# Performance work log

Measured on AMD Instinct MI355X. Metric: run time of the kernel, lower is better.

The kernel has to match this reference:

```python
import jax, jax.numpy as jnp
import numpy as np

N = 50000   # nodes
E = 400000  # edges
IN = 64     # input feature dim
H = 4       # heads (layers 1-2)
C = 128     # hidden channels per head
NEG_SLOPE = 0.2


def gat_conv(x, W, a_src, a_dst, b, src, dst, num_nodes):
    """PyG-style GATConv (add_self_loops=False, dropout inactive / eval mode).
    x: [N, F_in]; W: [F_in, H*C]; a_src/a_dst: [H, C]; b: [H*C].
    Returns concat-over-heads output [N, H*C]."""
    h = (x @ W).reshape(num_nodes, a_src.shape[0], a_src.shape[1])  # [N,H,C]
    alpha_s = jnp.einsum('nhc,hc->nh', h, a_src)  # [N,H]
    alpha_d = jnp.einsum('nhc,hc->nh', h, a_dst)  # [N,H]
    e = jax.nn.leaky_relu(alpha_s[src] + alpha_d[dst], NEG_SLOPE)  # [E,H]
    # numerically-stable segment softmax over incoming edges of each dst node
    m = jax.ops.segment_max(e, dst, num_segments=num_nodes)       # [N,H]
    m = jnp.where(jnp.isfinite(m), m, 0.0)                        # empty segments
    p = jnp.exp(e - m[dst])                                       # [E,H]
    denom = jax.ops.segment_sum(p, dst, num_segments=num_nodes)   # [N,H]
    alpha = p / (denom[dst] + 1e-16)                              # [E,H]
    # message = alpha * h[src], scatter-add into dst
    out = jax.ops.segment_sum(alpha[:, :, None] * h[src], dst,
                              num_segments=num_nodes)             # [N,H,C]
    return out.reshape(num_nodes, -1) + b


def setup_inputs() -> dict:
    key = jax.random.key(0)
    ks = jax.random.split(key, 16)
    s = 0.1  # weight scale for stability
    inp = {
        'x': jax.random.normal(ks[0], (N, IN), dtype=jnp.float32),
        'edge_index': jax.random.randint(ks[1], (2, E), 0, N, dtype=jnp.int64),
        # layer 1: 64 -> H*C
        'W1': s * jax.random.normal(ks[2], (IN, H * C), dtype=jnp.float32),
        'a_src1': s * jax.random.normal(ks[3], (H, C), dtype=jnp.float32),
        'a_dst1': s * jax.random.normal(ks[4], (H, C), dtype=jnp.float32),
        'b1': jnp.zeros((H * C,), dtype=jnp.float32),
        # layer 2: H*C -> H*C
        'W2': s * jax.random.normal(ks[5], (H * C, H * C), dtype=jnp.float32),
        'a_src2': s * jax.random.normal(ks[6], (H, C), dtype=jnp.float32),
        'a_dst2': s * jax.random.normal(ks[7], (H, C), dtype=jnp.float32),
        'b2': jnp.zeros((H * C,), dtype=jnp.float32),
        # layer 3: H*C -> C (heads=1)
        'W3': s * jax.random.normal(ks[8], (H * C, C), dtype=jnp.float32),
        'a_src3': s * jax.random.normal(ks[9], (1, C), dtype=jnp.float32),
        'a_dst3': s * jax.random.normal(ks[10], (1, C), dtype=jnp.float32),
        'b3': jnp.zeros((C,), dtype=jnp.float32),
    }
    return inp


def reference(x, edge_index, W1, a_src1, a_dst1, b1, W2, a_src2, a_dst2, b2,
              W3, a_src3, a_dst3, b3):
    src, dst = edge_index[0], edge_index[1]
    h = jax.nn.elu(gat_conv(x, W1, a_src1, a_dst1, b1, src, dst, N))
    h = jax.nn.elu(gat_conv(h, W2, a_src2, a_dst2, b2, src, dst, N))
    h = jax.nn.elu(gat_conv(h, W3, a_src3, a_dst3, b3, src, dst, N))
    return h  # [N, C]
```

## Files before the change

### kernel.cpp

```cpp
#include <hip/hip_runtime.h>
#include <math.h>


#define LRELU_SLOPE 0.2f
#define MPAD 50048

typedef __attribute__((ext_vector_type(8))) short short8;
typedef __attribute__((ext_vector_type(4))) float f32x4;

__device__ __forceinline__ float bf2f(unsigned short u) {
    return __uint_as_float(((unsigned int)u) << 16);
}
__device__ __forceinline__ unsigned short f2bf(float f) {
    unsigned int u = __float_as_uint(f);
    unsigned int r = u + 0x7FFFu + ((u >> 16) & 1u);
    return (unsigned short)(r >> 16);
}
__device__ __forceinline__ void load16_to_lds(const void* g, void* l) {
    __builtin_amdgcn_global_load_lds(
        (const __attribute__((address_space(1))) void*)g,
        (__attribute__((address_space(3))) void*)l, 16, 0, 0);
}
__device__ __forceinline__ float lrelu(float e) {
    return e > 0.f ? e : LRELU_SLOPE * e;
}


__global__ void count_deg_kernel(const int* __restrict__ dst, int* __restrict__ counts, int E) {
    int e = blockIdx.x * blockDim.x + threadIdx.x;
    if (e < E) atomicAdd(&counts[dst[e]], 1);
}

__global__ __launch_bounds__(1024) void scan1_kernel(const int* __restrict__ counts,
                                                     int* __restrict__ row_ptr,
                                                     int* __restrict__ partial, int n) {
    __shared__ int wsum[16];
    const int t = threadIdx.x;
    const int lane = t & 63, w = t >> 6;
    const int i = blockIdx.x * 1024 + t;
    int v = (i < n) ? counts[i] : 0;
    int s = v;
    #pragma unroll
    for (int off = 1; off < 64; off <<= 1) {
        int u = __shfl_up(s, off);
        if (lane >= off) s += u;
    }
    if (lane == 63) wsum[w] = s;
    __syncthreads();
    if (w == 0 && lane < 16) {
        int tv = wsum[lane];
        #pragma unroll
        for (int off = 1; off < 16; off <<= 1) {
            int u = __shfl_up(tv, off);
            if (lane >= off) tv += u;
        }
        wsum[lane] = tv;
    }
    __syncthreads();
    int incl = s + (w > 0 ? wsum[w - 1] : 0);
    if (i < n) row_ptr[i + 1] = incl;
    if (t == 0) partial[blockIdx.x] = wsum[15];
}

__global__ void scan2_kernel(int* __restrict__ partial, int nb) {
    int lane = threadIdx.x;
    int v = (lane < nb) ? partial[lane] : 0;
    int s = v;
    #pragma unroll
    for (int off = 1; off < 64; off <<= 1) {
        int u = __shfl_up(s, off);
        if (lane >= off) s += u;
    }
    if (lane < nb) partial[lane] = s - v;
}

__global__ __launch_bounds__(1024) void scan3_kernel(int* __restrict__ row_ptr,
                                                     const int* __restrict__ partial, int n) {
    const int i = blockIdx.x * 1024 + threadIdx.x;
    if (i < n) row_ptr[i + 1] += partial[blockIdx.x];
    if (i == 0) row_ptr[0] = 0;
}

__global__ void init_cursor_kernel(const int* __restrict__ row_ptr, int* __restrict__ cursor, int n) {
    int i = blockIdx.x * blockDim.x + threadIdx.x;
    if (i < n) cursor[i] = row_ptr[i];
}

__global__ void fill_csr_kernel(const int* __restrict__ src, const int* __restrict__ dst,
                                int* __restrict__ cursor, int* __restrict__ csr_src,
                                int* __restrict__ csr_dst, int E) {
    int e = blockIdx.x * blockDim.x + threadIdx.x;
    if (e < E) {
        int d = dst[e];
        int pos = atomicAdd(&cursor[d], 1);
        csr_src[pos] = src[e];
        csr_dst[pos] = d;
    }
}


__global__ void cast_f32_bf16_kernel(const float* __restrict__ in, unsigned short* __restrict__ out,
                                     size_t n) {
    size_t i = (size_t)blockIdx.x * blockDim.x + threadIdx.x;
    if (i < n) out[i] = f2bf(in[i]);
}

__global__ void transpose_cast_kernel(const float* __restrict__ W, unsigned short* __restrict__ Wt,
                                      int K, int Nw) {
    int i = blockIdx.x * blockDim.x + threadIdx.x;
    if (i < K * Nw) {
        int k = i / Nw, nn = i % Nw;
        Wt[(size_t)nn * K + k] = f2bf(W[i]);
    }
}


__global__ __launch_bounds__(256) void gemm_mfma_kernel(
    const unsigned short* __restrict__ A,
    const unsigned short* __restrict__ Bt,
    unsigned short* __restrict__ C,
    const float* __restrict__ a_src,
    const float* __restrict__ a_dst,
    float* __restrict__ als,
    float* __restrict__ ald,
    int M, int N, int K, int H)
{
    __shared__ short As[2 * 128 * 32];
    __shared__ short Bs[2 * 128 * 32];
    const int t = threadIdx.x;
    const int w = t >> 6, lane = t & 63;
    const int wr = w >> 1, wc = w & 1;

    const int nwg = gridDim.x * gridDim.y;
    const int wg  = blockIdx.x + gridDim.x * blockIdx.y;
    const int qch = nwg >> 3, rch = nwg & 7;
    const int xcd = wg & 7, pos = wg >> 3;
    const int lg  = (xcd < rch ? xcd * (qch + 1) : rch * (qch + 1) + (xcd - rch) * qch) + pos;
    const int bx  = lg % gridDim.x;
    const int by  = lg / gridDim.x;

    const int rowBase = by * 128;
    const int colBase = bx * 128;
    const int q = lane >> 4;
    const int r16 = lane & 15;
    const int qs = (q ^ ((r16 >> 1) & 3)) * 8;

    f32x4 acc[4][4] = {};

    const int sRow = t >> 2;
    const int sOff = ((t & 3) ^ ((sRow >> 1) & 3)) * 8;

    const int NT = K >> 5;
    auto stage = [&](int kt, int b) {
        const int koff = kt * 32 + sOff;
        #pragma unroll
        for (int rr = 0; rr < 2; ++rr) {
            const unsigned short* gA = A + (size_t)(rowBase + rr * 64 + sRow) * K + koff;
            load16_to_lds(gA, (char*)As + b * 8192 + rr * 4096 + w * 1024);
            const unsigned short* gB = Bt + (size_t)(colBase + rr * 64 + sRow) * K + koff;
            load16_to_lds(gB, (char*)Bs + b * 8192 + rr * 4096 + w * 1024);
        }
    };

    stage(0, 0);
    __syncthreads();

    for (int kt = 0; kt < NT; ++kt) {
        const int cur = kt & 1;
        if (kt + 1 < NT) stage(kt + 1, cur ^ 1);

        const short* Ab = As + cur * 4096;
        const short* Bb = Bs + cur * 4096;
        short8 af[4], bfr[4];
        #pragma unroll
        for (int m = 0; m < 4; ++m)
            af[m] = *(const short8*)&Ab[(wr * 64 + m * 16 + r16) * 32 + qs];
        #pragma unroll
        for (int n = 0; n < 4; ++n)
            bfr[n] = *(const short8*)&Bb[(wc * 64 + n * 16 + r16) * 32 + qs];
        #pragma unroll
        for (int m = 0; m < 4; ++m)
            #pragma unroll
            for (int n = 0; n < 4; ++n)
                acc[m][n] = __builtin_amdgcn_mfma_f32_16x16x32_bf16(af[m], bfr[n], acc[m][n], 0, 0, 0);

        __syncthreads();
    }

    float asv[4], adv[4];
    #pragma unroll
    for (int n = 0; n < 4; ++n) {
        int col = colBase + wc * 64 + n * 16 + r16;
        asv[n] = a_src[col];
        adv[n] = a_dst[col];
    }
    const int head = bx;

    float* red = (float*)As;

    #pragma unroll
    for (int m = 0; m < 4; ++m) {
        #pragma unroll
        for (int r = 0; r < 4; ++r) {
            const int rowl = wr * 64 + m * 16 + q * 4 + r;
            const int gr = rowBase + rowl;
            float ps = 0.f, pd = 0.f;
            #pragma unroll
            for (int n = 0; n < 4; ++n) {
                ps += acc[m][n][r] * asv[n];
                pd += acc[m][n][r] * adv[n];
            }
            #pragma unroll
            for (int off = 8; off >= 1; off >>= 1) {
                ps += __shfl_xor(ps, off);
                pd += __shfl_xor(pd, off);
            }
            if (r16 == 0) {
                red[wc * 128 + rowl] = ps;
                red[256 + wc * 128 + rowl] = pd;
            }
            if (gr < M) {
                #pragma unroll
                for (int n = 0; n < 4; ++n)
                    C[(size_t)gr * N + colBase + wc * 64 + n * 16 + r16] = f2bf(acc[m][n][r]);
            }
        }
    }
    __syncthreads();
    if (t < 128) {
        const int gr = rowBase + t;
        if (gr < M) {
            als[(size_t)gr * H + head] = red[t] + red[128 + t];
            ald[(size_t)gr * H + head] = red[256 + t] + red[384 + t];
        }
    }
}


template <int H>
__global__ __launch_bounds__(256) void edge_w_kernel(
    const int* __restrict__ csr_src, const int* __restrict__ csr_dst,
    const float* __restrict__ als, const float* __restrict__ ald,
    float* __restrict__ wplane, int E)
{
    int p = blockIdx.x * 256 + threadIdx.x;
    if (p >= E) return;
    int s = csr_src[p], d = csr_dst[p];
    if constexpr (H == 4) {
        float4 a = *(const float4*)&als[(size_t)s * 4];
        float4 b = *(const float4*)&ald[(size_t)d * 4];
        wplane[p]               = __expf(lrelu(a.x + b.x));
        wplane[(size_t)E + p]   = __expf(lrelu(a.y + b.y));
        wplane[2*(size_t)E + p] = __expf(lrelu(a.z + b.z));
        wplane[3*(size_t)E + p] = __expf(lrelu(a.w + b.w));
    } else {
        wplane[p] = __expf(lrelu(als[s] + ald[d]));
    }
}


__global__ __launch_bounds__(256) void gather4_kernel(
    const unsigned short* __restrict__ hfeat,
    const float* __restrict__ wplane,
    const int* __restrict__ row_ptr, const int* __restrict__ csr_src,
    const float* __restrict__ bias, unsigned short* __restrict__ out,
    int E, int n_nodes)
{
    const int lane = threadIdx.x & 63;
    const int wv = threadIdx.x >> 6;
    const int n = blockIdx.x * 4 + wv;
    if (n >= n_nodes) return;
    const int head = lane >> 4;
    const int li = lane & 15;
    const int grpBase = lane & ~15;

    const int start = row_ptr[n];
    const int deg = row_ptr[n + 1] - start;
    const float* wpl = wplane + (size_t)head * E;

    float acc[8] = {};
    float wsum = 0.f;
    for (int base = 0; base < deg; base += 16) {
        const int cnt = min(16, deg - base);
        int s_l = 0; float w_l = 0.f;
        if (li < cnt) {
            s_l = csr_src[start + base + li];
            w_l = wpl[start + base + li];
            wsum += w_l;
        }
        for (int e = 0; e < cnt; ++e) {
            const int s = __shfl(s_l, grpBase + e);
            const float a = __shfl(w_l, grpBase + e);
            short8 v = *(const short8*)(hfeat + (size_t)s * 512 + lane * 8);
            #pragma unroll
            for (int j = 0; j < 8; ++j) acc[j] += a * bf2f((unsigned short)v[j]);
        }
    }

    #pragma unroll
    for (int off = 8; off >= 1; off >>= 1) wsum += __shfl_xor(wsum, off);
    const float sc = (deg > 0) ? 1.f / wsum : 0.f;

    float ov[8];
    #pragma unroll
    for (int j = 0; j < 8; ++j) {
        float o = acc[j] * sc + bias[lane * 8 + j];
        ov[j] = o > 0.f ? o : expm1f(o);
    }
    short8 v;
    #pragma unroll
    for (int j = 0; j < 8; ++j) v[j] = (short)f2bf(ov[j]);
    *(short8*)&out[(size_t)n * 512 + lane * 8] = v;
}


__global__ __launch_bounds__(256) void gather1_kernel(
    const unsigned short* __restrict__ hfeat,
    const float* __restrict__ wplane,
    const int* __restrict__ row_ptr, const int* __restrict__ csr_src,
    const float* __restrict__ bias, float* __restrict__ out, int n_nodes)
{
    const int lane = threadIdx.x & 63;
    const int wv = threadIdx.x >> 6;
    const int n = blockIdx.x * 4 + wv;
    if (n >= n_nodes) return;
    const int qid = lane >> 4;
    const int ql = lane & 15;

    const int start = row_ptr[n];
    const int deg = row_ptr[n + 1] - start;

    float acc[8] = {};
    float wsum = 0.f;
    for (int base = 0; base < deg; base += 64) {
        const int cnt = min(64, deg - base);
        int s_l = 0; float w_l = 0.f;
        if (lane < cnt) {
            s_l = csr_src[start + base + lane];
            w_l = wplane[start + base + lane];
            wsum += w_l;
        }
        for (int e = 0; e < cnt; e += 4) {
            const int idx = e + qid;
            const int idxc = idx < cnt ? idx : 0;
            const int s = __shfl(s_l, idxc);
            const float aw = __shfl(w_l, idxc);
            const float a = idx < cnt ? aw : 0.f;
            short8 v = *(const short8*)(hfeat + (size_t)s * 128 + ql * 8);
            #pragma unroll
            for (int j = 0; j < 8; ++j) acc[j] += a * bf2f((unsigned short)v[j]);
        }
    }

    #pragma unroll
    for (int off = 32; off >= 1; off >>= 1) wsum += __shfl_xor(wsum, off);
    const float sc = (deg > 0) ? 1.f / wsum : 0.f;

    #pragma unroll
    for (int j = 0; j < 8; ++j) {
        acc[j] += __shfl_xor(acc[j], 16);
        acc[j] += __shfl_xor(acc[j], 32);
    }

    if (qid == 0) {
        float tmp[8];
        #pragma unroll
        for (int j = 0; j < 8; ++j) {
            float o = acc[j] * sc + bias[ql * 8 + j];
            tmp[j] = o > 0.f ? o : expm1f(o);
        }
        float4 o0 = {tmp[0], tmp[1], tmp[2], tmp[3]};
        float4 o1 = {tmp[4], tmp[5], tmp[6], tmp[7]};
        float* op = out + (size_t)n * 128 + ql * 8;
        *(float4*)op = o0;
        *(float4*)(op + 4) = o1;
    }
}


extern "C" void kernel_launch(void* const* d_in, const int* in_sizes, int n_in,
                              void* d_out, int out_size, void* d_ws, size_t ws_size,
                              hipStream_t stream) {
    const float* x   = (const float*)d_in[0];
    const int*   ei  = (const int*)d_in[1];
    const float* W1  = (const float*)d_in[2];
    const float* as1 = (const float*)d_in[3];
    const float* ad1 = (const float*)d_in[4];
    const float* b1  = (const float*)d_in[5];
    const float* W2  = (const float*)d_in[6];
    const float* as2 = (const float*)d_in[7];
    const float* ad2 = (const float*)d_in[8];
    const float* b2  = (const float*)d_in[9];
    const float* W3  = (const float*)d_in[10];
    const float* as3 = (const float*)d_in[11];
    const float* ad3 = (const float*)d_in[12];
    const float* b3  = (const float*)d_in[13];

    const int N = in_sizes[0] / 64;
    const int E = in_sizes[1] / 2;
    const int HC = 512;

    const int* src = ei;
    const int* dst = ei + E;

    size_t off = 0;
    auto carve = [&](size_t bytes) -> void* {
        void* p = (char*)d_ws + off;
        off += (bytes + 255) & ~(size_t)255;
        return p;
    };
    unsigned short* x_bf    = (unsigned short*)carve((size_t)MPAD * 64 * 2);
    unsigned short* feat_bf = (unsigned short*)carve((size_t)MPAD * HC * 2);
    unsigned short* h_bf    = (unsigned short*)carve((size_t)N * HC * 2);
    unsigned short* W1t     = (unsigned short*)carve((size_t)512 * 64 * 2);
    unsigned short* W2t     = (unsigned short*)carve((size_t)512 * 512 * 2);
    unsigned short* W3t     = (unsigned short*)carve((size_t)128 * 512 * 2);
    float* stats  = (float*)carve((size_t)N * 8 * sizeof(float));
    float* als    = stats;
    float* ald    = stats + (size_t)N * 4;
    float* wplane = (float*)carve((size_t)4 * E * sizeof(float));
    int*   counts = (int*)carve((size_t)N * sizeof(int));
    int*   row_ptr= (int*)carve((size_t)(N + 1) * sizeof(int));
    int*   cursor = (int*)carve((size_t)N * sizeof(int));
    int*   csr_src= (int*)carve((size_t)E * sizeof(int));
    int*   csr_dst= (int*)carve((size_t)E * sizeof(int));
    int*   partial= (int*)carve(64 * sizeof(int));
    (void)ws_size;

    const int nb = (N + 1023) / 1024;

    hipMemsetAsync(counts, 0, (size_t)N * sizeof(int), stream);
    count_deg_kernel<<<(E + 255) / 256, 256, 0, stream>>>(dst, counts, E);
    scan1_kernel<<<nb, 1024, 0, stream>>>(counts, row_ptr, partial, N);
    scan2_kernel<<<1, 64, 0, stream>>>(partial, nb);
    scan3_kernel<<<nb, 1024, 0, stream>>>(row_ptr, partial, N);
    init_cursor_kernel<<<(N + 255) / 256, 256, 0, stream>>>(row_ptr, cursor, N);
    fill_csr_kernel<<<(E + 255) / 256, 256, 0, stream>>>(src, dst, cursor, csr_src, csr_dst, E);

    cast_f32_bf16_kernel<<<((size_t)N * 64 + 255) / 256, 256, 0, stream>>>(x, x_bf, (size_t)N * 64);
    transpose_cast_kernel<<<(64 * 512 + 255) / 256, 256, 0, stream>>>(W1, W1t, 64, 512);
    transpose_cast_kernel<<<(512 * 512 + 255) / 256, 256, 0, stream>>>(W2, W2t, 512, 512);
    transpose_cast_kernel<<<(512 * 128 + 255) / 256, 256, 0, stream>>>(W3, W3t, 512, 128);

    const int rowTiles = (N + 127) / 128;
    const int aggBlocks = (N + 3) / 4;
    const int edgeBlocks = (E + 255) / 256;

    gemm_mfma_kernel<<<dim3(4, rowTiles), 256, 0, stream>>>(x_bf, W1t, h_bf, as1, ad1,
                                                            als, ald, N, 512, 64, 4);
    edge_w_kernel<4><<<edgeBlocks, 256, 0, stream>>>(csr_src, csr_dst, als, ald, wplane, E);
    gather4_kernel<<<aggBlocks, 256, 0, stream>>>(h_bf, wplane, row_ptr, csr_src,
                                                  b1, feat_bf, E, N);

    gemm_mfma_kernel<<<dim3(4, rowTiles), 256, 0, stream>>>(feat_bf, W2t, h_bf, as2, ad2,
                                                            als, ald, N, 512, 512, 4);
    edge_w_kernel<4><<<edgeBlocks, 256, 0, stream>>>(csr_src, csr_dst, als, ald, wplane, E);
    gather4_kernel<<<aggBlocks, 256, 0, stream>>>(h_bf, wplane, row_ptr, csr_src,
                                                  b2, feat_bf, E, N);

    gemm_mfma_kernel<<<dim3(1, rowTiles), 256, 0, stream>>>(feat_bf, W3t, h_bf, as3, ad3,
                                                            als, ald, N, 128, 512, 1);
    edge_w_kernel<1><<<edgeBlocks, 256, 0, stream>>>(csr_src, csr_dst, als, ald, wplane, E);
    gather1_kernel<<<aggBlocks, 256, 0, stream>>>(h_bf, wplane, row_ptr, csr_src,
                                                  b3, (float*)d_out, N);
}
```

Baseline: 383.2 us.

## Reorder layer-1 GAT as aggregate-then-project using folded attention weights

Layer 1 now folds W1 into the attention vectors, so the per-node attention logits come straight from the 64-dim input. It then aggregates the raw 64-dim inputs per head and runs a small GEMM with fused bias and ELU afterwards. This replaces gathering 512-wide projected features with gathering 64-wide inputs, which cuts edge-gather traffic for the first layer. Edge weights are also stored as interleaved float4 per edge instead of separate head planes. The cost is an extra aggregated buffer and a per-head GEMM, and the logits now use fp32 x while the features use bf16, so rounding differs slightly from before.

```diff
diff --git a/kernel.cpp b/kernel.cpp
--- a/kernel.cpp
+++ b/kernel.cpp
@@ -111,6 +111,244 @@
     if (i < K * Nw) {
         int k = i / Nw, nn = i % Nw;
         Wt[(size_t)nn * K + k] = f2bf(W[i]);
+    }
+}
+
+
+__global__ __launch_bounds__(256) void ws1_kernel(const float* __restrict__ W1,
+                                                  const float* __restrict__ as1,
+                                                  const float* __restrict__ ad1,
+                                                  float* __restrict__ ws) {
+    const int t = threadIdx.x;
+    const int h = t >> 6, k = t & 63;
+    float ss = 0.f, sd = 0.f;
+    for (int c = 0; c < 128; ++c) {
+        float wv = W1[k * 512 + h * 128 + c];
+        ss += wv * as1[h * 128 + c];
+        sd += wv * ad1[h * 128 + c];
+    }
+    ws[h * 64 + k] = ss;
+    ws[256 + h * 64 + k] = sd;
+}
+
+
+__global__ __launch_bounds__(256) void als1_kernel(const float* __restrict__ x,
+                                                   const float* __restrict__ ws,
+                                                   float* __restrict__ als,
+                                                   float* __restrict__ ald, int n_nodes) {
+    const int lane = threadIdx.x & 63;
+    const int wv = threadIdx.x >> 6;
+    const int n = blockIdx.x * 4 + wv;
+    if (n >= n_nodes) return;
+    const float xv = x[(size_t)n * 64 + lane];
+    float d0 = xv * ws[lane],        d1 = xv * ws[64 + lane];
+    float d2 = xv * ws[128 + lane],  d3 = xv * ws[192 + lane];
+    float e0 = xv * ws[256 + lane],  e1 = xv * ws[320 + lane];
+    float e2 = xv * ws[384 + lane],  e3 = xv * ws[448 + lane];
+    #pragma unroll
+    for (int off = 32; off >= 1; off >>= 1) {
+        d0 += __shfl_xor(d0, off); d1 += __shfl_xor(d1, off);
+        d2 += __shfl_xor(d2, off); d3 += __shfl_xor(d3, off);
+        e0 += __shfl_xor(e0, off); e1 += __shfl_xor(e1, off);
+        e2 += __shfl_xor(e2, off); e3 += __shfl_xor(e3, off);
+    }
+    if (lane == 0) {
+        float4 a = {d0, d1, d2, d3};
+        float4 b = {e0, e1, e2, e3};
+        *(float4*)&als[(size_t)n * 4] = a;
+        *(float4*)&ald[(size_t)n * 4] = b;
+    }
+}
+
+
+__global__ __launch_bounds__(256) void edge_w4_kernel(
+    const int* __restrict__ csr_src, const int* __restrict__ csr_dst,
+    const float* __restrict__ als, const float* __restrict__ ald,
+    float4* __restrict__ wplane4, int E)
+{
+    int p = blockIdx.x * 256 + threadIdx.x;
+    if (p >= E) return;
+    int s = csr_src[p], d = csr_dst[p];
+    float4 a = *(const float4*)&als[(size_t)s * 4];
+    float4 b = *(const float4*)&ald[(size_t)d * 4];
+    float4 o;
+    o.x = __expf(lrelu(a.x + b.x));
+    o.y = __expf(lrelu(a.y + b.y));
+    o.z = __expf(lrelu(a.z + b.z));
+    o.w = __expf(lrelu(a.w + b.w));
+    wplane4[p] = o;
+}
+
+__global__ __launch_bounds__(256) void edge_w1_kernel(
+    const int* __restrict__ csr_src, const int* __restrict__ csr_dst,
+    const float* __restrict__ als, const float* __restrict__ ald,
+    float* __restrict__ wplane, int E)
+{
+    int p = blockIdx.x * 256 + threadIdx.x;
+    if (p >= E) return;
+    wplane[p] = __expf(lrelu(als[csr_src[p]] + ald[csr_dst[p]]));
+}
+
+
+__global__ __launch_bounds__(256) void gatherx_kernel(
+    const unsigned short* __restrict__ x_bf,
+    const float4* __restrict__ wplane4,
+    const int* __restrict__ row_ptr, const int* __restrict__ csr_src,
+    unsigned short* __restrict__ xagg,
+    int n_nodes)
+{
+    const int lane = threadIdx.x & 63;
+    const int wv = threadIdx.x >> 6;
+    const int n = blockIdx.x * 4 + wv;
+    if (n >= n_nodes) return;
+    const int g = lane >> 3;
+    const int j = lane & 7;
+
+    const int start = row_ptr[n];
+    const int deg = row_ptr[n + 1] - start;
+
+    float acc[4][8] = {};
+    float asum[4] = {};
+
+    for (int base = 0; base < deg; base += 8) {
+        const int idx = base + g;
+        const bool ok = idx < deg;
+        const int p = start + (ok ? idx : 0);
+        const int s = csr_src[p];
+        float4 a4 = wplane4[p];
+        if (!ok) { a4.x = 0.f; a4.y = 0.f; a4.z = 0.f; a4.w = 0.f; }
+        short8 v = *(const short8*)(x_bf + (size_t)s * 64 + j * 8);
+        asum[0] += a4.x; asum[1] += a4.y; asum[2] += a4.z; asum[3] += a4.w;
+        #pragma unroll
+        for (int jj = 0; jj < 8; ++jj) {
+            const float xv = bf2f((unsigned short)v[jj]);
+            acc[0][jj] += a4.x * xv;
+            acc[1][jj] += a4.y * xv;
+            acc[2][jj] += a4.z * xv;
+            acc[3][jj] += a4.w * xv;
+        }
+    }
+
+    #pragma unroll
+    for (int h = 0; h < 4; ++h) {
+        asum[h] += __shfl_xor(asum[h], 8);
+        asum[h] += __shfl_xor(asum[h], 16);
+        asum[h] += __shfl_xor(asum[h], 32);
+        #pragma unroll
+        for (int jj = 0; jj < 8; ++jj) {
+            acc[h][jj] += __shfl_xor(acc[h][jj], 8);
+            acc[h][jj] += __shfl_xor(acc[h][jj], 16);
+            acc[h][jj] += __shfl_xor(acc[h][jj], 32);
+        }
+    }
+
+    if (lane < 32) {
+        const int h = g;
+        float sc = 0.f;
+        if (deg > 0) {
+            float av = (h == 0) ? asum[0] : (h == 1) ? asum[1] : (h == 2) ? asum[2] : asum[3];
+            sc = 1.f / av;
+        }
+        short8 o;
+        #pragma unroll
+        for (int jj = 0; jj < 8; ++jj) {
+            float val = ((h == 0) ? acc[0][jj] : (h == 1) ? acc[1][jj]
+                        : (h == 2) ? acc[2][jj] : acc[3][jj]) * sc;
+            o[jj] = (short)f2bf(val);
+        }
+        *(short8*)&xagg[(size_t)n * 256 + h * 64 + j * 8] = o;
+    }
+}
+
+
+__global__ __launch_bounds__(256) void gemm_out_kernel(
+    const unsigned short* __restrict__ A,
+    const unsigned short* __restrict__ Bt,
+    const float* __restrict__ bias,
+    unsigned short* __restrict__ Cout,
+    int M)
+{
+    __shared__ short As[2 * 128 * 32];
+    __shared__ short Bs[2 * 128 * 32];
+    const int t = threadIdx.x;
+    const int w = t >> 6, lane = t & 63;
+    const int wr = w >> 1, wc = w & 1;
+
+    const int nwg = gridDim.x * gridDim.y;
+    const int wg  = blockIdx.x + gridDim.x * blockIdx.y;
+    const int qch = nwg >> 3, rch = nwg & 7;
+    const int xcd = wg & 7, pos = wg >> 3;
+    const int lg  = (xcd < rch ? xcd * (qch + 1) : rch * (qch + 1) + (xcd - rch) * qch) + pos;
+    const int bx  = lg % gridDim.x;
+    const int by  = lg / gridDim.x;
+
+    const int rowBase = by * 128;
+    const int head = bx;
+    const int colBase = bx * 128;
+    const int q = lane >> 4;
+    const int r16 = lane & 15;
+    const int qs = (q ^ ((r16 >> 1) & 3)) * 8;
+
+    f32x4 acc[4][4] = {};
+
+    const int sRow = t >> 2;
+    const int sOff = ((t & 3) ^ ((sRow >> 1) & 3)) * 8;
+
+    auto stage = [&](int kt, int b) {
+        const int koff = kt * 32 + sOff;
+        #pragma unroll
+        for (int rr = 0; rr < 2; ++rr) {
+            const unsigned short* gA = A + (size_t)(rowBase + rr * 64 + sRow) * 256 + head * 64 + koff;
+            load16_to_lds(gA, (char*)As + b * 8192 + rr * 4096 + w * 1024);
+            const unsigned short* gB = Bt + (size_t)(colBase + rr * 64 + sRow) * 64 + koff;
+            load16_to_lds(gB, (char*)Bs + b * 8192 + rr * 4096 + w * 1024);
+        }
+    };
+
+    stage(0, 0);
+    __syncthreads();
+
+    #pragma unroll
+    for (int kt = 0; kt < 2; ++kt) {
+        const int cur = kt & 1;
+        if (kt + 1 < 2) stage(kt + 1, cur ^ 1);
+
+        const short* Ab = As + cur * 4096;
+        const short* Bb = Bs + cur * 4096;
+        short8 af[4], bfr[4];
+        #pragma unroll
+        for (int m = 0; m < 4; ++m)
+            af[m] = *(const short8*)&Ab[(wr * 64 + m * 16 + r16) * 32 + qs];
+        #pragma unroll
+        for (int n = 0; n < 4; ++n)
+            bfr[n] = *(const short8*)&Bb[(wc * 64 + n * 16 + r16) * 32 + qs];
+        #pragma unroll
+        for (int m = 0; m < 4; ++m)
+            #pragma unroll
+            for (int n = 0; n < 4; ++n)
+                acc[m][n] = __builtin_amdgcn_mfma_f32_16x16x32_bf16(af[m], bfr[n], acc[m][n], 0, 0, 0);
+
+        __syncthreads();
+    }
+
+    float bv[4];
+    #pragma unroll
+    for (int n = 0; n < 4; ++n) bv[n] = bias[colBase + wc * 64 + n * 16 + r16];
+
+    #pragma unroll
+    for (int m = 0; m < 4; ++m) {
+        #pragma unroll
+        for (int r = 0; r < 4; ++r) {
+            const int gr = rowBase + wr * 64 + m * 16 + q * 4 + r;
+            if (gr < M) {
+                #pragma unroll
+                for (int n = 0; n < 4; ++n) {
+                    float o = acc[m][n][r] + bv[n];
+                    o = o > 0.f ? o : expm1f(o);
+                    Cout[(size_t)gr * 512 + colBase + wc * 64 + n * 16 + r16] = f2bf(o);
+                }
+            }
+        }
     }
 }
 
@@ -237,34 +475,12 @@
 }
 
 
-template <int H>
-__global__ __launch_bounds__(256) void edge_w_kernel(
-    const int* __restrict__ csr_src, const int* __restrict__ csr_dst,
-    const float* __restrict__ als, const float* __restrict__ ald,
-    float* __restrict__ wplane, int E)
-{
-    int p = blockIdx.x * 256 + threadIdx.x;
-    if (p >= E) return;
-    int s = csr_src[p], d = csr_dst[p];
-    if constexpr (H == 4) {
-        float4 a = *(const float4*)&als[(size_t)s * 4];
-        float4 b = *(const float4*)&ald[(size_t)d * 4];
-        wplane[p]               = __expf(lrelu(a.x + b.x));
-        wplane[(size_t)E + p]   = __expf(lrelu(a.y + b.y));
-        wplane[2*(size_t)E + p] = __expf(lrelu(a.z + b.z));
-        wplane[3*(size_t)E + p] = __expf(lrelu(a.w + b.w));
-    } else {
-        wplane[p] = __expf(lrelu(als[s] + ald[d]));
-    }
-}
-
-
 __global__ __launch_bounds__(256) void gather4_kernel(
     const unsigned short* __restrict__ hfeat,
-    const float* __restrict__ wplane,
+    const float4* __restrict__ wplane4,
     const int* __restrict__ row_ptr, const int* __restrict__ csr_src,
     const float* __restrict__ bias, unsigned short* __restrict__ out,
-    int E, int n_nodes)
+    int n_nodes)
 {
     const int lane = threadIdx.x & 63;
     const int wv = threadIdx.x >> 6;
@@ -276,7 +492,6 @@
 
     const int start = row_ptr[n];
     const int deg = row_ptr[n + 1] - start;
-    const float* wpl = wplane + (size_t)head * E;
 
     float acc[8] = {};
     float wsum = 0.f;
@@ -285,7 +500,8 @@
         int s_l = 0; float w_l = 0.f;
         if (li < cnt) {
             s_l = csr_src[start + base + li];
-            w_l = wpl[start + base + li];
+            float4 w4 = wplane4[start + base + li];
+            w_l = (head == 0) ? w4.x : (head == 1) ? w4.y : (head == 2) ? w4.z : w4.w;
             wsum += w_l;
         }
         for (int e = 0; e < cnt; ++e) {
@@ -412,13 +628,16 @@
     unsigned short* x_bf    = (unsigned short*)carve((size_t)MPAD * 64 * 2);
     unsigned short* feat_bf = (unsigned short*)carve((size_t)MPAD * HC * 2);
     unsigned short* h_bf    = (unsigned short*)carve((size_t)N * HC * 2);
+    unsigned short* xagg    = (unsigned short*)carve((size_t)MPAD * 256 * 2);
     unsigned short* W1t     = (unsigned short*)carve((size_t)512 * 64 * 2);
     unsigned short* W2t     = (unsigned short*)carve((size_t)512 * 512 * 2);
     unsigned short* W3t     = (unsigned short*)carve((size_t)128 * 512 * 2);
     float* stats  = (float*)carve((size_t)N * 8 * sizeof(float));
     float* als    = stats;
     float* ald    = stats + (size_t)N * 4;
-    float* wplane = (float*)carve((size_t)4 * E * sizeof(float));
+    float4* wplane4 = (float4*)carve((size_t)E * sizeof(float4));
+    float* wplane1  = (float*)carve((size_t)E * sizeof(float));
+    float* ws     = (float*)carve(512 * sizeof(float));
     int*   counts = (int*)carve((size_t)N * sizeof(int));
     int*   row_ptr= (int*)carve((size_t)(N + 1) * sizeof(int));
     int*   cursor = (int*)carve((size_t)N * sizeof(int));
@@ -441,26 +660,26 @@
     transpose_cast_kernel<<<(64 * 512 + 255) / 256, 256, 0, stream>>>(W1, W1t, 64, 512);
     transpose_cast_kernel<<<(512 * 512 + 255) / 256, 256, 0, stream>>>(W2, W2t, 512, 512);
     transpose_cast_kernel<<<(512 * 128 + 255) / 256, 256, 0, stream>>>(W3, W3t, 512, 128);
+    ws1_kernel<<<1, 256, 0, stream>>>(W1, as1, ad1, ws);
 
     const int rowTiles = (N + 127) / 128;
     const int aggBlocks = (N + 3) / 4;
     const int edgeBlocks = (E + 255) / 256;
 
-    gemm_mfma_kernel<<<dim3(4, rowTiles), 256, 0, stream>>>(x_bf, W1t, h_bf, as1, ad1,
-                                                            als, ald, N, 512, 64, 4);
-    edge_w_kernel<4><<<edgeBlocks, 256, 0, stream>>>(csr_src, csr_dst, als, ald, wplane, E);
-    gather4_kernel<<<aggBlocks, 256, 0, stream>>>(h_bf, wplane, row_ptr, csr_src,
-                                                  b1, feat_bf, E, N);
+    als1_kernel<<<aggBlocks, 256, 0, stream>>>(x, ws, als, ald, N);
+    edge_w4_kernel<<<edgeBlocks, 256, 0, stream>>>(csr_src, csr_dst, als, ald, wplane4, E);
+    gatherx_kernel<<<aggBlocks, 256, 0, stream>>>(x_bf, wplane4, row_ptr, csr_src, xagg, N);
+    gemm_out_kernel<<<dim3(4, rowTiles), 256, 0, stream>>>(xagg, W1t, b1, feat_bf, N);
 
     gemm_mfma_kernel<<<dim3(4, rowTiles), 256, 0, stream>>>(feat_bf, W2t, h_bf, as2, ad2,
                                                             als, ald, N, 512, 512, 4);
-    edge_w_kernel<4><<<edgeBlocks, 256, 0, stream>>>(csr_src, csr_dst, als, ald, wplane, E);
-    gather4_kernel<<<aggBlocks, 256, 0, stream>>>(h_bf, wplane, row_ptr, csr_src,
-                                                  b2, feat_bf, E, N);
+    edge_w4_kernel<<<edgeBlocks, 256, 0, stream>>>(csr_src, csr_dst, als, ald, wplane4, E);
+    gather4_kernel<<<aggBlocks, 256, 0, stream>>>(h_bf, wplane4, row_ptr, csr_src,
+                                                  b2, feat_bf, N);
 
     gemm_mfma_kernel<<<dim3(1, rowTiles), 256, 0, stream>>>(feat_bf, W3t, h_bf, as3, ad3,
                                                             als, ald, N, 128, 512, 1);
-    edge_w_kernel<1><<<edgeBlocks, 256, 0, stream>>>(csr_src, csr_dst, als, ald, wplane, E);
-    gather1_kernel<<<aggBlocks, 256, 0, stream>>>(h_bf, wplane, row_ptr, csr_src,
+    edge_w1_kernel<<<edgeBlocks, 256, 0, stream>>>(csr_src, csr_dst, als, ald, wplane1, E);
+    gather1_kernel<<<aggBlocks, 256, 0, stream>>>(h_bf, wplane1, row_ptr, csr_src,
                                                   b3, (float*)d_out, N);
 }
```

Result: slower. 402.0 us (+4.9%).

## Fuse edge-weight computation into gather kernels and merge preprocessing launches

Applied to the files above, without the earlier changes.

Removes the separate edge_w kernels and their wplane buffer, so each gather now computes the exp(leaky_relu(als[src]+ald[dst])) weights inline from per-node scores. The cast, transpose and counts-zeroing launches are folded into one prep kernel, and cursor initialisation moves into the scan3 kernel, so csr_dst is no longer built. This cuts kernel launches and avoids writing and re-reading the per-edge weight planes. In exchange the gather recomputes exp per head per edge and does scattered reads into als.

```diff
diff --git a/kernel.cpp b/kernel.cpp
--- a/kernel.cpp
+++ b/kernel.cpp
@@ -23,6 +23,39 @@
 }
 __device__ __forceinline__ float lrelu(float e) {
     return e > 0.f ? e : LRELU_SLOPE * e;
+}
+
+
+__global__ __launch_bounds__(256) void prep_kernel(
+    const float* __restrict__ x, const float* __restrict__ W1,
+    const float* __restrict__ W2, const float* __restrict__ W3,
+    unsigned short* __restrict__ x_bf, unsigned short* __restrict__ W1t,
+    unsigned short* __restrict__ W2t, unsigned short* __restrict__ W3t,
+    int* __restrict__ counts, int N)
+{
+    int i = blockIdx.x * 256 + threadIdx.x;
+    const int nx = N * 64;
+    if (i < nx) { x_bf[i] = f2bf(x[i]); return; }
+    i -= nx;
+    if (i < 64 * 512) {
+        int k = i / 512, nn = i % 512;
+        W1t[nn * 64 + k] = f2bf(W1[i]);
+        return;
+    }
+    i -= 64 * 512;
+    if (i < 512 * 512) {
+        int k = i / 512, nn = i % 512;
+        W2t[nn * 512 + k] = f2bf(W2[i]);
+        return;
+    }
+    i -= 512 * 512;
+    if (i < 512 * 128) {
+        int k = i / 128, nn = i % 128;
+        W3t[(size_t)nn * 512 + k] = f2bf(W3[i]);
+        return;
+    }
+    i -= 512 * 128;
+    if (i < N) counts[i] = 0;
 }
 
 
@@ -74,43 +107,26 @@
     if (lane < nb) partial[lane] = s - v;
 }
 
-__global__ __launch_bounds__(1024) void scan3_kernel(int* __restrict__ row_ptr,
-                                                     const int* __restrict__ partial, int n) {
+__global__ __launch_bounds__(1024) void scan3c_kernel(int* __restrict__ row_ptr,
+                                                      const int* __restrict__ partial,
+                                                      const int* __restrict__ counts,
+                                                      int* __restrict__ cursor, int n) {
     const int i = blockIdx.x * 1024 + threadIdx.x;
-    if (i < n) row_ptr[i + 1] += partial[blockIdx.x];
+    if (i < n) {
+        int rp1 = row_ptr[i + 1] + partial[blockIdx.x];
+        row_ptr[i + 1] = rp1;
+        cursor[i] = rp1 - counts[i];
+    }
     if (i == 0) row_ptr[0] = 0;
 }
 
-__global__ void init_cursor_kernel(const int* __restrict__ row_ptr, int* __restrict__ cursor, int n) {
-    int i = blockIdx.x * blockDim.x + threadIdx.x;
-    if (i < n) cursor[i] = row_ptr[i];
-}
-
 __global__ void fill_csr_kernel(const int* __restrict__ src, const int* __restrict__ dst,
-                                int* __restrict__ cursor, int* __restrict__ csr_src,
-                                int* __restrict__ csr_dst, int E) {
+                                int* __restrict__ cursor, int* __restrict__ csr_src, int E) {
     int e = blockIdx.x * blockDim.x + threadIdx.x;
     if (e < E) {
         int d = dst[e];
         int pos = atomicAdd(&cursor[d], 1);
         csr_src[pos] = src[e];
-        csr_dst[pos] = d;
-    }
-}
-
-
-__global__ void cast_f32_bf16_kernel(const float* __restrict__ in, unsigned short* __restrict__ out,
-                                     size_t n) {
-    size_t i = (size_t)blockIdx.x * blockDim.x + threadIdx.x;
-    if (i < n) out[i] = f2bf(in[i]);
-}
-
-__global__ void transpose_cast_kernel(const float* __restrict__ W, unsigned short* __restrict__ Wt,
-                                      int K, int Nw) {
-    int i = blockIdx.x * blockDim.x + threadIdx.x;
-    if (i < K * Nw) {
-        int k = i / Nw, nn = i % Nw;
-        Wt[(size_t)nn * K + k] = f2bf(W[i]);
     }
 }
 
@@ -237,34 +253,12 @@
 }
 
 
-template <int H>
-__global__ __launch_bounds__(256) void edge_w_kernel(
-    const int* __restrict__ csr_src, const int* __restrict__ csr_dst,
+__global__ __launch_bounds__(256) void gather4f_kernel(
+    const unsigned short* __restrict__ hfeat,
     const float* __restrict__ als, const float* __restrict__ ald,
-    float* __restrict__ wplane, int E)
-{
-    int p = blockIdx.x * 256 + threadIdx.x;
-    if (p >= E) return;
-    int s = csr_src[p], d = csr_dst[p];
-    if constexpr (H == 4) {
-        float4 a = *(const float4*)&als[(size_t)s * 4];
-        float4 b = *(const float4*)&ald[(size_t)d * 4];
-        wplane[p]               = __expf(lrelu(a.x + b.x));
-        wplane[(size_t)E + p]   = __expf(lrelu(a.y + b.y));
-        wplane[2*(size_t)E + p] = __expf(lrelu(a.z + b.z));
-        wplane[3*(size_t)E + p] = __expf(lrelu(a.w + b.w));
-    } else {
-        wplane[p] = __expf(lrelu(als[s] + ald[d]));
-    }
-}
-
-
-__global__ __launch_bounds__(256) void gather4_kernel(
-    const unsigned short* __restrict__ hfeat,
-    const float* __restrict__ wplane,
     const int* __restrict__ row_ptr, const int* __restrict__ csr_src,
     const float* __restrict__ bias, unsigned short* __restrict__ out,
-    int E, int n_nodes)
+    int n_nodes)
 {
     const int lane = threadIdx.x & 63;
     const int wv = threadIdx.x >> 6;
@@ -276,7 +270,7 @@
 
     const int start = row_ptr[n];
     const int deg = row_ptr[n + 1] - start;
-    const float* wpl = wplane + (size_t)head * E;
+    const float aldv = ald[(size_t)n * 4 + head];
 
     float acc[8] = {};
     float wsum = 0.f;
@@ -285,7 +279,8 @@
         int s_l = 0; float w_l = 0.f;
         if (li < cnt) {
             s_l = csr_src[start + base + li];
-            w_l = wpl[start + base + li];
+            float e = als[(size_t)s_l * 4 + head] + aldv;
+            w_l = __expf(lrelu(e));
             wsum += w_l;
         }
         for (int e = 0; e < cnt; ++e) {
@@ -314,9 +309,9 @@
 }
 
 
-__global__ __launch_bounds__(256) void gather1_kernel(
+__global__ __launch_bounds__(256) void gather1f_kernel(
     const unsigned short* __restrict__ hfeat,
-    const float* __restrict__ wplane,
+    const float* __restrict__ als, const float* __restrict__ ald,
     const int* __restrict__ row_ptr, const int* __restrict__ csr_src,
     const float* __restrict__ bias, float* __restrict__ out, int n_nodes)
 {
@@ -329,6 +324,7 @@
 
     const int start = row_ptr[n];
     const int deg = row_ptr[n + 1] - start;
+    const float aldv = ald[n];
 
     float acc[8] = {};
     float wsum = 0.f;
@@ -337,7 +333,8 @@
         int s_l = 0; float w_l = 0.f;
         if (lane < cnt) {
             s_l = csr_src[start + base + lane];
-            w_l = wplane[start + base + lane];
+            float e = als[s_l] + aldv;
+            w_l = __expf(lrelu(e));
             wsum += w_l;
         }
         for (int e = 0; e < cnt; e += 4) {
@@ -418,49 +415,40 @@
     float* stats  = (float*)carve((size_t)N * 8 * sizeof(float));
     float* als    = stats;
     float* ald    = stats + (size_t)N * 4;
-    float* wplane = (float*)carve((size_t)4 * E * sizeof(float));
     int*   counts = (int*)carve((size_t)N * sizeof(int));
     int*   row_ptr= (int*)carve((size_t)(N + 1) * sizeof(int));
     int*   cursor = (int*)carve((size_t)N * sizeof(int));
     int*   csr_src= (int*)carve((size_t)E * sizeof(int));
-    int*   csr_dst= (int*)carve((size_t)E * sizeof(int));
     int*   partial= (int*)carve(64 * sizeof(int));
     (void)ws_size;
 
     const int nb = (N + 1023) / 1024;
-
-    hipMemsetAsync(counts, 0, (size_t)N * sizeof(int), stream);
+    const int prepTotal = N * 64 + 64 * 512 + 512 * 512 + 512 * 128 + N;
+
+    prep_kernel<<<(prepTotal + 255) / 256, 256, 0, stream>>>(
+        x, W1, W2, W3, x_bf, W1t, W2t, W3t, counts, N);
+
     count_deg_kernel<<<(E + 255) / 256, 256, 0, stream>>>(dst, counts, E);
     scan1_kernel<<<nb, 1024, 0, stream>>>(counts, row_ptr, partial, N);
     scan2_kernel<<<1, 64, 0, stream>>>(partial, nb);
-    scan3_kernel<<<nb, 1024, 0, stream>>>(row_ptr, partial, N);
-    init_cursor_kernel<<<(N + 255) / 256, 256, 0, stream>>>(row_ptr, cursor, N);
-    fill_csr_kernel<<<(E + 255) / 256, 256, 0, stream>>>(src, dst, cursor, csr_src, csr_dst, E);
-
-    cast_f32_bf16_kernel<<<((size_t)N * 64 + 255) / 256, 256, 0, stream>>>(x, x_bf, (size_t)N * 64);
-    transpose_cast_kernel<<<(64 * 512 + 255) / 256, 256, 0, stream>>>(W1, W1t, 64, 512);
-    transpose_cast_kernel<<<(512 * 512 + 255) / 256, 256, 0, stream>>>(W2, W2t, 512, 512);
-    transpose_cast_kernel<<<(512 * 128 + 255) / 256, 256, 0, stream>>>(W3, W3t, 512, 128);
+    scan3c_kernel<<<nb, 1024, 0, stream>>>(row_ptr, partial, counts, cursor, N);
+    fill_csr_kernel<<<(E + 255) / 256, 256, 0, stream>>>(src, dst, cursor, csr_src, E);
 
     const int rowTiles = (N + 127) / 128;
     const int aggBlocks = (N + 3) / 4;
-    const int edgeBlocks = (E + 255) / 256;
 
     gemm_mfma_kernel<<<dim3(4, rowTiles), 256, 0, stream>>>(x_bf, W1t, h_bf, as1, ad1,
                                                             als, ald, N, 512, 64, 4);
-    edge_w_kernel<4><<<edgeBlocks, 256, 0, stream>>>(csr_src, csr_dst, als, ald, wplane, E);
-    gather4_kernel<<<aggBlocks, 256, 0, stream>>>(h_bf, wplane, row_ptr, csr_src,
-                                                  b1, feat_bf, E, N);
+    gather4f_kernel<<<aggBlocks, 256, 0, stream>>>(h_bf, als, ald, row_ptr, csr_src,
+                                                   b1, feat_bf, N);
 
     gemm_mfma_kernel<<<dim3(4, rowTiles), 256, 0, stream>>>(feat_bf, W2t, h_bf, as2, ad2,
                                                             als, ald, N, 512, 512, 4);
-    edge_w_kernel<4><<<edgeBlocks, 256, 0, stream>>>(csr_src, csr_dst, als, ald, wplane, E);
-    gather4_kernel<<<aggBlocks, 256, 0, stream>>>(h_bf, wplane, row_ptr, csr_src,
-                                                  b2, feat_bf, E, N);
+    gather4f_kernel<<<aggBlocks, 256, 0, stream>>>(h_bf, als, ald, row_ptr, csr_src,
+                                                   b2, feat_bf, N);
 
     gemm_mfma_kernel<<<dim3(1, rowTiles), 256, 0, stream>>>(feat_bf, W3t, h_bf, as3, ad3,
                                                             als, ald, N, 128, 512, 1);
-    edge_w_kernel<1><<<edgeBlocks, 256, 0, stream>>>(csr_src, csr_dst, als, ald, wplane, E);
-    gather1_kernel<<<aggBlocks, 256, 0, stream>>>(h_bf, wplane, row_ptr, csr_src,
-                                                  b3, (float*)d_out, N);
-}
+    gather1f_kernel<<<aggBlocks, 256, 0, stream>>>(h_bf, als, ald, row_ptr, csr_src,
+                                                   b3, (float*)d_out, N);
+}
```

Measured after the change: 359.4 us. 6.2% less time.
